# Kernel optimization log

Measured on AMD Instinct MI355X. Metric: run time of the kernel, lower is better.

## Reference

```python
import jax, jax.numpy as jnp
import numpy as np

H, W = 101, 31
HEADS, DH, FREQ = 8, 64, 64
C_DIM = 256
INNER = HEADS * DH
EPS = 1e-5


def _conv2d(x, w, b):
    # x: (B, Cin, H, W), w: (Cout, Cin, 3, 3) -> SAME padding, stride 1
    y = jax.lax.conv_general_dilated(x, w, (1, 1), 'SAME',
                                     dimension_numbers=('NCHW', 'OIHW', 'NCHW'))
    return y + b[None, :, None, None]


def setup_inputs() -> dict:
    key = jax.random.key(0)
    ks = jax.random.split(key, 8)
    B = 32
    N = H * W  # 3131
    s = 0.02
    x = jax.random.normal(ks[0], (B, N, C_DIM), jnp.float32)
    conv_fx_w = jax.random.normal(ks[1], (INNER, C_DIM, 3, 3), jnp.float32) * s
    conv_fx_b = jnp.zeros((INNER,), jnp.float32)
    conv_x_w = jax.random.normal(ks[2], (INNER, C_DIM, 3, 3), jnp.float32) * s
    conv_x_b = jnp.zeros((INNER,), jnp.float32)
    gate_w = jax.random.normal(ks[3], (FREQ, DH), jnp.float32) * s  # nn.Linear weight (out,in)
    gate_b = jnp.zeros((FREQ,), jnp.float32)
    temperature = jnp.full((1, HEADS, 1, 1), 0.5, jnp.float32)
    ln_gamma = jnp.ones((FREQ, DH), jnp.float32)
    ln_beta = jnp.zeros((FREQ, DH), jnp.float32)
    mlp_w = jax.random.normal(ks[4], (DH, DH), jnp.float32) * s
    out_w = jax.random.normal(ks[5], (C_DIM, INNER), jnp.float32) * s
    out_b = jnp.zeros((C_DIM,), jnp.float32)
    # fixed (non-trainable) spectral basis, L2-normalized per row like F.normalize(dim=-1)
    inver = jax.random.normal(ks[6], (N, FREQ), jnp.float32)
    inver = inver / jnp.linalg.norm(inver, axis=-1, keepdims=True)
    return dict(x=x, conv_fx_w=conv_fx_w, conv_fx_b=conv_fx_b, conv_x_w=conv_x_w,
                conv_x_b=conv_x_b, gate_w=gate_w, gate_b=gate_b,
                temperature=temperature, ln_gamma=ln_gamma, ln_beta=ln_beta,
                mlp_w=mlp_w, out_w=out_w, out_b=out_b, inver=inver)


def reference(x, conv_fx_w, conv_fx_b, conv_x_w, conv_x_b, gate_w, gate_b,
              temperature, ln_gamma, ln_beta, mlp_w, out_w, out_b, inver):
    B, N, C = x.shape
    xi = x.reshape(B, H, W, C).transpose(0, 3, 1, 2)  # (B, C, H, W)

    def proj(w, b):
        y = _conv2d(xi, w, b)                                  # (B, inner, H, W)
        return y.transpose(0, 2, 3, 1).reshape(B, N, HEADS, DH).transpose(0, 2, 1, 3)  # (B,h,N,d)

    fx_mid = proj(conv_fx_w, conv_fx_b)
    x_mid = proj(conv_x_w, conv_x_b)

    temp = jnp.clip(temperature, 0.1, 5.0)                      # (1,h,1,1)
    logits = jnp.einsum('bhnc,gc->bhng', x_mid, gate_w) + gate_b
    gate = jax.nn.softmax(logits / temp, axis=-1)               # (B,h,N,g)
    eigens = gate * inver[None, None]                           # (B,h,N,g)

    spec = jnp.einsum('bhnc,bhng->bhgc', fx_mid, eigens)        # (B,h,g,c)
    # LayerNorm over the trailing (g, c) axes jointly
    mu = spec.mean(axis=(-2, -1), keepdims=True)
    var = spec.var(axis=(-2, -1), keepdims=True)
    spec = (spec - mu) * jax.lax.rsqrt(var + EPS) * ln_gamma + ln_beta

    out_spec = jnp.einsum('bhgi,io->bhgo', spec, mlp_w)
    out_x = jnp.einsum('bhgc,bhng->bhnc', out_spec, eigens)     # (B,h,N,c)
    out_x = out_x.transpose(0, 2, 1, 3).reshape(B, N, HEADS * DH)
    return jnp.einsum('bnd,cd->bnc', out_x, out_w) + out_b      # to_out (dropout is identity)
```

## Files before the change

kernel.cpp:

```cpp
#include <hip/hip_runtime.h>
#include <hip/hip_bf16.h>
#include <stdint.h>

#define HH 101
#define WW 31
#define NN 3131
#define NPAD 3136
#define BB 32
#define NH 8
#define CDIM 256
#define GG 64
#define HP 103
#define WP 33

typedef __attribute__((ext_vector_type(8))) short bf16x8;
typedef __attribute__((ext_vector_type(4))) float f32x4;
typedef __attribute__((ext_vector_type(4))) unsigned short ushort4_t;
typedef __attribute__((ext_vector_type(8))) unsigned short ushort8_t;
typedef __attribute__((ext_vector_type(4))) float float4_t;

static __device__ __forceinline__ unsigned short f2bf(float f) {
  union { float f; uint32_t u; } v; v.f = f;
  uint32_t u = v.u;
  return (unsigned short)((u + 0x7fffu + ((u >> 16) & 1u)) >> 16);
}
static __device__ __forceinline__ float bf2f(unsigned short h) {
  union { uint32_t u; float f; } v; v.u = ((uint32_t)h) << 16;
  return v.f;
}
static __device__ __forceinline__ void gload_lds16(const void* g, void* l) {
  __builtin_amdgcn_global_load_lds((const __attribute__((address_space(1))) void*)g,
                                   (__attribute__((address_space(3))) void*)l, 16, 0, 0);
}
static __device__ __forceinline__ int xcd_swz(int bid, int nwg) {
  int q = nwg >> 3, r = nwg & 7;
  int xcd = bid & 7, pos = bid >> 3;
  int base = (xcd < r) ? xcd * (q + 1) : r * (q + 1) + (xcd - r) * q;
  return base + pos;
}

__global__ void k_pad(const float* __restrict__ x, unsigned short* __restrict__ xpad, int b0) {
  const int xx = blockIdx.x, yy = blockIdx.y, b = blockIdx.z;
  const int t = threadIdx.x;
  ushort4_t o; o.x = 0; o.y = 0; o.z = 0; o.w = 0;
  if (yy >= 1 && yy <= HH && xx >= 1 && xx <= WW) {
    const int n = (yy - 1) * WW + (xx - 1);
    const float4_t v = *(const float4_t*)(x + (((int64_t)(b0 + b) * NN + n) * CDIM + t * 4));
    o.x = f2bf(v.x); o.y = f2bf(v.y); o.z = f2bf(v.z); o.w = f2bf(v.w);
  }
  *(ushort4_t*)(xpad + (((int64_t)b * HP + yy) * WP + xx) * CDIM + t * 4) = o;
}

__global__ void k_wpack(const float* __restrict__ fxw, const float* __restrict__ xw,
                        const float* __restrict__ fxb, const float* __restrict__ xb,
                        const float* __restrict__ gw,
                        unsigned short* __restrict__ Wb, float* __restrict__ bias,
                        unsigned short* __restrict__ gwb) {
  int tid = blockIdx.x * blockDim.x + threadIdx.x;
  const int total = 9 * 1024 * 256;
  if (tid < total) {
    int cin = tid & 255; int rest = tid >> 8; int co = rest & 1023; int t = rest >> 10;
    float v = (co < 512) ? fxw[(int64_t)co * 2304 + cin * 9 + t]
                         : xw[(int64_t)(co - 512) * 2304 + cin * 9 + t];
    Wb[tid] = f2bf(v);
  }
  if (tid < 1024) bias[tid] = (tid < 512) ? fxb[tid] : xb[tid - 512];
  if (tid < 4096) gwb[tid] = f2bf(gw[tid]);
}

__global__ void k_pprep(const float* __restrict__ mlp, const float* __restrict__ outw,
                        unsigned short* __restrict__ Pt) {
  int h = blockIdx.x >> 6, i = blockIdx.x & 63, co = threadIdx.x;
  float a = 0.f;
  for (int c = 0; c < 64; ++c) a += mlp[i * 64 + c] * outw[(int64_t)co * 512 + h * 64 + c];
  Pt[((int64_t)h * 256 + co) * 64 + i] = f2bf(a);
}

__global__ void k_padzero(unsigned short* __restrict__ fxT, unsigned short* __restrict__ xmid,
                          int CB) {
  int tid = blockIdx.x * blockDim.x + threadIdx.x;
  if (tid >= CB * 2560) return;
  {
    int j = tid % 5; int rc = tid / 5;
    fxT[(int64_t)rc * NPAD + NN + j] = 0;
  }
  {
    int d = tid & 63; int rest = tid >> 6;
    int j = rest % 5; int bh = rest / 5;
    xmid[((int64_t)bh * NPAD + NN + j) * 64 + d] = 0;
  }
}

__launch_bounds__(512, 2)
__global__ void k_conv8(const unsigned short* __restrict__ xpad,
                        const unsigned short* __restrict__ Wb,
                        const float* __restrict__ bias,
                        unsigned short* __restrict__ fxT,
                        unsigned short* __restrict__ xmid) {
  extern __shared__ unsigned short lds[];
  const int swz = xcd_swz(blockIdx.x, gridDim.x);
  const int r   = swz % 52;
  const int b   = swz / 52;
  const int bx  = r & 3;
  const int mt  = r >> 2;
  const int tid = threadIdx.x, wid = tid >> 6, lane = tid & 63;
  const int wm = wid & 3, wn = wid >> 2;
  const int arow = lane & 15, col16 = lane >> 4;
  const int n00 = mt * 256, co00 = bx * 256;

  const int srow = wid * 16 + (lane >> 2);
  const int tc   = ((lane & 3) ^ ((lane >> 3) & 3)) * 8;
  int na0 = n00 + srow;        if (na0 >= NN) na0 = NN - 1;
  int na1 = n00 + srow + 128;  if (na1 >= NN) na1 = NN - 1;
  const int y0 = na0 / WW, x0v = na0 % WW;
  const int y1 = na1 / WW, x1v = na1 % WW;
  const unsigned short* aS0 = xpad + ((int64_t)(b * HP + y0) * WP + x0v) * CDIM + tc;
  const unsigned short* aS1 = xpad + ((int64_t)(b * HP + y1) * WP + x1v) * CDIM + tc;
  const unsigned short* bS0 = Wb + (int64_t)(co00 + srow) * CDIM + tc;
  const unsigned short* bS1 = Wb + (int64_t)(co00 + srow + 128) * CDIM + tc;

  const int rdsz = (col16 ^ ((arow >> 1) & 3)) * 8;

  f32x4 acc[4][8] = {};
  bf16x8 a0[4], a1[4], b03[4], b47[4];

#define STAGE_A(s, kk, aoffv)                                        \
  { unsigned short* d = lds + (s) * 32768 + (kk) * 8192 + wid * 512; \
    gload_lds16(aS0 + (aoffv) + (kk) * 32, d);                       \
    gload_lds16(aS1 + (aoffv) + (kk) * 32, d + 4096); }
#define STAGE_B(s, kk, boffv)                                                \
  { unsigned short* d = lds + (s) * 32768 + 16384 + (kk) * 8192 + wid * 512; \
    gload_lds16(bS0 + (boffv) + (kk) * 32, d);                               \
    gload_lds16(bS1 + (boffv) + (kk) * 32, d + 4096); }
#define KOFF(ks, aoffv, boffv)                              \
  { const int tap = (ks) >> 2;                              \
    const int dy = (tap >= 6) + (tap >= 3);                 \
    const int dx = tap - dy * 3;                            \
    const int cb = ((ks) & 3) << 6;                         \
    aoffv = (dy * WP + dx) * CDIM + cb;                     \
    boffv = tap * 262144 + cb; }
#define RD_A(dst, s, kk, mf)                                                             \
  dst = *(const bf16x8*)(lds + (s) * 32768 + (kk) * 8192 +                               \
                         (wm * 64 + (mf) * 16 + arow) * 32 + rdsz);
#define RD_B(dst, s, kk, nf)                                                             \
  dst = *(const bf16x8*)(lds + (s) * 32768 + 16384 + (kk) * 8192 +                       \
                         (wn * 128 + (nf) * 16 + arow) * 32 + rdsz);
#define MFMA16(aset, bset, nbase)                                                        \
  __builtin_amdgcn_s_setprio(1);                                                         \
  _Pragma("unroll")                                                                      \
  for (int mf = 0; mf < 4; ++mf) {                                                       \
    _Pragma("unroll")                                                                    \
    for (int nf = 0; nf < 4; ++nf)                                                       \
      acc[mf][(nbase) + nf] =                                                            \
        __builtin_amdgcn_mfma_f32_16x16x32_bf16(aset[mf], bset[nf], acc[mf][(nbase) + nf], 0, 0, 0); \
  }                                                                                      \
  __builtin_amdgcn_s_setprio(0);

  int aoff0, boff0;
  KOFF(0, aoff0, boff0);
  STAGE_A(0, 0, aoff0); STAGE_B(0, 0, boff0);
  STAGE_A(0, 1, aoff0); STAGE_B(0, 1, boff0);
  asm volatile("s_waitcnt vmcnt(4)" ::: "memory");
  __builtin_amdgcn_s_barrier();
  asm volatile("" ::: "memory");
  #pragma unroll
  for (int i = 0; i < 4; ++i) { RD_A(a0[i], 0, 0, i); }
  #pragma unroll
  for (int i = 0; i < 4; ++i) { RD_B(b03[i], 0, 0, i); }

  #pragma unroll 1
  for (int t = 0; t < 36; ++t) {
    const int cur = t & 1, nxt = cur ^ 1;
    const int tn = (t < 35) ? t + 1 : 35;
    int aoffn, boffn;
    KOFF(tn, aoffn, boffn);

    #pragma unroll
    for (int i = 0; i < 4; ++i) { RD_B(b47[i], cur, 0, 4 + i); }
    STAGE_A(nxt, 0, aoffn);
    asm volatile("s_waitcnt lgkmcnt(4)" ::: "memory");
    __builtin_amdgcn_sched_barrier(0);
    MFMA16(a0, b03, 0);

    STAGE_B(nxt, 0, boffn);
    asm volatile("s_waitcnt vmcnt(4)" ::: "memory");
    __builtin_amdgcn_s_barrier();
    asm volatile("" ::: "memory");
    #pragma unroll
    for (int i = 0; i < 4; ++i) { RD_A(a1[i], cur, 1, i); }
    #pragma unroll
    for (int i = 0; i < 4; ++i) { RD_B(b03[i], cur, 1, i); }
    asm volatile("s_waitcnt lgkmcnt(8)" ::: "memory");
    __builtin_amdgcn_sched_barrier(0);
    MFMA16(a0, b47, 4);

    #pragma unroll
    for (int i = 0; i < 4; ++i) { RD_B(b47[i], cur, 1, 4 + i); }
    STAGE_A(nxt, 1, aoffn);
    asm volatile("s_waitcnt lgkmcnt(4)" ::: "memory");
    __builtin_amdgcn_sched_barrier(0);
    MFMA16(a1, b03, 0);

    STAGE_B(nxt, 1, boffn);
    asm volatile("s_waitcnt vmcnt(4)" ::: "memory");
    __builtin_amdgcn_s_barrier();
    asm volatile("" ::: "memory");
    #pragma unroll
    for (int i = 0; i < 4; ++i) { RD_A(a0[i], nxt, 0, i); }
    #pragma unroll
    for (int i = 0; i < 4; ++i) { RD_B(b03[i], nxt, 0, i); }
    asm volatile("s_waitcnt lgkmcnt(8)" ::: "memory");
    __builtin_amdgcn_sched_barrier(0);
    MFMA16(a1, b47, 4);
  }

  asm volatile("s_waitcnt vmcnt(0) lgkmcnt(0)" ::: "memory");

  const int rowoff = col16 * 4;
  #pragma unroll
  for (int mf = 0; mf < 4; ++mf) {
    const int nr = n00 + wm * 64 + mf * 16 + rowoff;
    #pragma unroll
    for (int nf = 0; nf < 8; ++nf) {
      const int co = co00 + wn * 128 + nf * 16 + arow;
      const float bvs = bias[co];
      const float v0 = acc[mf][nf][0] + bvs;
      const float v1 = acc[mf][nf][1] + bvs;
      const float v2 = acc[mf][nf][2] + bvs;
      const float v3 = acc[mf][nf][3] + bvs;
      if (bx < 2) {
        const int h = co >> 6, c = co & 63;
        unsigned short* dst = fxT + ((int64_t)((b * NH + h) * 64 + c)) * NPAD + nr;
        if (nr + 3 < NN) {
          ushort4_t o; o.x = f2bf(v0); o.y = f2bf(v1); o.z = f2bf(v2); o.w = f2bf(v3);
          *(ushort4_t*)dst = o;
        } else {
          if (nr + 0 < NN) dst[0] = f2bf(v0);
          if (nr + 1 < NN) dst[1] = f2bf(v1);
          if (nr + 2 < NN) dst[2] = f2bf(v2);
          if (nr + 3 < NN) dst[3] = f2bf(v3);
        }
      } else {
        const int h = (co >> 6) & 7, d = co & 63;
        unsigned short* dst = xmid + ((int64_t)(b * NH + h) * NPAD + nr) * 64 + d;
        if (nr + 0 < NN) dst[0] = f2bf(v0);
        if (nr + 1 < NN) dst[64] = f2bf(v1);
        if (nr + 2 < NN) dst[128] = f2bf(v2);
        if (nr + 3 < NN) dst[192] = f2bf(v3);
      }
    }
  }
#undef STAGE_A
#undef STAGE_B
#undef KOFF
#undef RD_A
#undef RD_B
#undef MFMA16
}

__global__ void k_eig(const unsigned short* __restrict__ xmid,
                      const unsigned short* __restrict__ gwb,
                      const float* __restrict__ gateb,
                      const float* __restrict__ temperature,
                      const float* __restrict__ inver,
                      unsigned short* __restrict__ eigT,
                      unsigned short* __restrict__ eigN) {
  __shared__ unsigned short egN[64 * 72];
  __shared__ unsigned short egT[64 * 72];
  const int nt = blockIdx.x, h = blockIdx.y, b = blockIdx.z;
  const int tid = threadIdx.x;
  const int w = tid >> 6, lane = tid & 63;
  const int n0 = nt * 64 + w * 16;
  const int bh = b * NH + h;
  float tv = temperature[h];
  tv = fminf(fmaxf(tv, 0.1f), 5.0f);
  const float itemp = 1.0f / tv;
  const int arow = lane & 15;
  const int koff = (lane >> 4) * 8;
  const unsigned short* aptr = xmid + ((int64_t)bh * NPAD + (n0 + arow)) * 64 + koff;
  bf16x8 a0 = *(const bf16x8*)(aptr);
  bf16x8 a1 = *(const bf16x8*)(aptr + 32);
  f32x4 acc[4] = {};
  #pragma unroll
  for (int ng = 0; ng < 4; ++ng) {
    const unsigned short* bptr = gwb + (ng * 16 + arow) * 64 + koff;
    bf16x8 b0 = *(const bf16x8*)(bptr);
    bf16x8 b1 = *(const bf16x8*)(bptr + 32);
    acc[ng] = __builtin_amdgcn_mfma_f32_16x16x32_bf16(a0, b0, acc[ng], 0, 0, 0);
    acc[ng] = __builtin_amdgcn_mfma_f32_16x16x32_bf16(a1, b1, acc[ng], 0, 0, 0);
  }
  #pragma unroll
  for (int r = 0; r < 4; ++r) {
    const int nl = w * 16 + ((lane >> 4) << 2) + r;
    const int n = nt * 64 + nl;
    float vals[4];
    #pragma unroll
    for (int ng = 0; ng < 4; ++ng) vals[ng] = (acc[ng][r] + gateb[ng * 16 + arow]) * itemp;
    float mx = fmaxf(fmaxf(vals[0], vals[1]), fmaxf(vals[2], vals[3]));
    #pragma unroll
    for (int s = 1; s < 16; s <<= 1) mx = fmaxf(mx, __shfl_xor(mx, s));
    float ex[4]; float sum = 0.f;
    #pragma unroll
    for (int ng = 0; ng < 4; ++ng) { ex[ng] = __expf(vals[ng] - mx); sum += ex[ng]; }
    #pragma unroll
    for (int s = 1; s < 16; s <<= 1) sum += __shfl_xor(sum, s);
    const float inv = 1.0f / sum;
    const bool valid = (n < NN);
    #pragma unroll
    for (int ng = 0; ng < 4; ++ng) {
      const int g = ng * 16 + arow;
      float iv = valid ? inver[(int64_t)n * GG + g] : 0.f;
      unsigned short u = valid ? f2bf(ex[ng] * inv * iv) : (unsigned short)0;
      egN[nl * 72 + g] = u;
      egT[g * 72 + nl] = u;
    }
  }
  __syncthreads();
  const int row = tid >> 2, c0 = (tid & 3) << 4;
  {
    ushort8_t v0 = *(ushort8_t*)&egN[row * 72 + c0];
    ushort8_t v1 = *(ushort8_t*)&egN[row * 72 + c0 + 8];
    unsigned short* dst = eigN + ((int64_t)bh * NPAD + nt * 64 + row) * 64 + c0;
    *(ushort8_t*)dst = v0; *(ushort8_t*)(dst + 8) = v1;
  }
  {
    ushort8_t v0 = *(ushort8_t*)&egT[row * 72 + c0];
    ushort8_t v1 = *(ushort8_t*)&egT[row * 72 + c0 + 8];
    unsigned short* dst = eigT + ((int64_t)(bh * 64 + row)) * NPAD + nt * 64 + c0;
    *(ushort8_t*)dst = v0; *(ushort8_t*)(dst + 8) = v1;
  }
}

__launch_bounds__(256, 1)
__global__ void k_specln(const unsigned short* __restrict__ eigT,
                         const unsigned short* __restrict__ fxT,
                         const float* __restrict__ gamma, const float* __restrict__ beta,
                         const unsigned short* __restrict__ Pt,
                         unsigned short* __restrict__ m2t) {
  extern __shared__ char sm[];
  float* sacc = (float*)sm;
  unsigned short* specb = (unsigned short*)(sm + 66560);
  float* red = (float*)(sm + 74752);
  unsigned short* mstrip = (unsigned short*)(sm + 74784);
  const int bhl = blockIdx.x;
  const int h = bhl & 7, bl = bhl >> 3;
  const int tid = threadIdx.x, w = tid >> 6, lane = tid & 63;
  const int arow = lane & 15, col16 = lane >> 4;
  const int koff = col16 * 8;
  const unsigned short* eb = eigT + (int64_t)bhl * 64 * NPAD;
  const unsigned short* fb = fxT + (int64_t)bhl * 64 * NPAD;

  const int ks0 = (98 * w) >> 2, ks1 = (98 * (w + 1)) >> 2;
  f32x4 acc[4][4] = {};
  for (int ks = ks0; ks < ks1; ++ks) {
    const int k0 = ks * 32 + koff;
    bf16x8 av[4], bv[4];
    #pragma unroll
    for (int mg = 0; mg < 4; ++mg) av[mg] = *(const bf16x8*)(eb + (int64_t)(mg * 16 + arow) * NPAD + k0);
    #pragma unroll
    for (int ng = 0; ng < 4; ++ng) bv[ng] = *(const bf16x8*)(fb + (int64_t)(ng * 16 + arow) * NPAD + k0);
    #pragma unroll
    for (int mg = 0; mg < 4; ++mg)
      #pragma unroll
      for (int ng = 0; ng < 4; ++ng)
        acc[mg][ng] = __builtin_amdgcn_mfma_f32_16x16x32_bf16(av[mg], bv[ng], acc[mg][ng], 0, 0, 0);
  }
  float* pw = sacc + w * (64 * 65);
  #pragma unroll
  for (int mg = 0; mg < 4; ++mg)
    #pragma unroll
    for (int ng = 0; ng < 4; ++ng)
      #pragma unroll
      for (int r = 0; r < 4; ++r)
        pw[(mg * 16 + col16 * 4 + r) * 65 + ng * 16 + arow] = acc[mg][ng][r];
  __syncthreads();

  float vloc[16];
  float lsum = 0.f, lsq = 0.f;
  #pragma unroll
  for (int idx = 0; idx < 16; ++idx) {
    const int e = tid + idx * 256;
    const int g = e >> 6, c = e & 63;
    float v = sacc[g * 65 + c] + sacc[4160 + g * 65 + c] +
              sacc[8320 + g * 65 + c] + sacc[12480 + g * 65 + c];
    vloc[idx] = v; lsum += v; lsq += v * v;
  }
  #pragma unroll
  for (int s = 1; s < 64; s <<= 1) { lsum += __shfl_xor(lsum, s); lsq += __shfl_xor(lsq, s); }
  if (lane == 0) { red[w] = lsum; red[4 + w] = lsq; }
  __syncthreads();
  const float tsum = red[0] + red[1] + red[2] + red[3];
  const float tsq = red[4] + red[5] + red[6] + red[7];
  const float mu = tsum * (1.0f / 4096.0f);
  const float var = tsq * (1.0f / 4096.0f) - mu * mu;
  const float rs = rsqrtf(var + 1e-5f);
  #pragma unroll
  for (int idx = 0; idx < 16; ++idx) {
    const int e = tid + idx * 256;
    const int g = e >> 6, c = e & 63;
    float sv = (vloc[idx] - mu) * rs * gamma[e] + beta[e];
    specb[g * 64 + ((((c >> 3) ^ (g & 7))) << 3) + (c & 7)] = f2bf(sv);
  }
  __syncthreads();

  f32x4 a2[4][4] = {};
  const unsigned short* pth = Pt + ((int64_t)h * 256 + w * 64) * 64;
  #pragma unroll
  for (int kk = 0; kk < 2; ++kk) {
    const int i0 = kk * 32 + koff;
    const int i8 = (i0 >> 3);
    bf16x8 av2[4], bv2[4];
    #pragma unroll
    for (int mg = 0; mg < 4; ++mg) {
      const int g = mg * 16 + arow;
      av2[mg] = *(const bf16x8*)(specb + g * 64 + ((i8 ^ (g & 7)) << 3));
    }
    #pragma unroll
    for (int ng = 0; ng < 4; ++ng)
      bv2[ng] = *(const bf16x8*)(pth + (ng * 16 + arow) * 64 + i0);
    #pragma unroll
    for (int mg = 0; mg < 4; ++mg)
      #pragma unroll
      for (int ng = 0; ng < 4; ++ng)
        a2[mg][ng] = __builtin_amdgcn_mfma_f32_16x16x32_bf16(av2[mg], bv2[ng], a2[mg][ng], 0, 0, 0);
  }
  unsigned short* ms = mstrip + w * (64 * 72);
  #pragma unroll
  for (int mg = 0; mg < 4; ++mg)
    #pragma unroll
    for (int ng = 0; ng < 4; ++ng)
      #pragma unroll
      for (int r = 0; r < 4; ++r)
        ms[(ng * 16 + arow) * 72 + mg * 16 + col16 * 4 + r] = f2bf(a2[mg][ng][r]);
  __syncthreads();
  #pragma unroll
  for (int e0 = 0; e0 < 8; ++e0) {
    const int e = lane + e0 * 64;
    const int row = e >> 3, g8 = e & 7;
    ushort8_t v = *(ushort8_t*)&ms[row * 72 + g8 * 8];
    *(ushort8_t*)(m2t + ((int64_t)(bl * 256 + w * 64 + row)) * 512 + h * 64 + g8 * 8) = v;
  }
}

__launch_bounds__(256)
__global__ void k_out(const unsigned short* __restrict__ eigN,
                      const unsigned short* __restrict__ m2t,
                      const float* __restrict__ outb,
                      float* __restrict__ out, int b0) {
  const int swz = xcd_swz(blockIdx.x, gridDim.x);
  const int ct = swz & 1;
  const int mt = (swz >> 1) % 25;
  const int b  = swz / 50;
  const int w = threadIdx.x >> 6, lane = threadIdx.x & 63;
  const int wm = w >> 1, wn = w & 1;
  const int arow = lane & 15, koff = (lane >> 4) * 8;
  const int co0 = ct * 128 + wn * 64;
  const int n0 = mt * 128 + wm * 64;
  f32x4 acc[4][4] = {};
  const unsigned short* ebase = eigN + (int64_t)b * NH * NPAD * 64;
  const unsigned short* mbase = m2t + (int64_t)b * 256 * 512;
  for (int ks = 0; ks < 16; ++ks) {
    const int hh = ks >> 1;
    const int g0 = (ks & 1) * 32 + koff;
    bf16x8 av[4], bv[4];
    #pragma unroll
    for (int mg = 0; mg < 4; ++mg) {
      int n = n0 + mg * 16 + arow;
      if (n > NPAD - 1) n = NPAD - 1;
      av[mg] = *(const bf16x8*)(ebase + ((int64_t)hh * NPAD + n) * 64 + g0);
    }
    #pragma unroll
    for (int ng = 0; ng < 4; ++ng)
      bv[ng] = *(const bf16x8*)(mbase + (int64_t)(co0 + ng * 16 + arow) * 512 + ks * 32 + koff);
    #pragma unroll
    for (int mg = 0; mg < 4; ++mg)
      #pragma unroll
      for (int ng = 0; ng < 4; ++ng)
        acc[mg][ng] = __builtin_amdgcn_mfma_f32_16x16x32_bf16(av[mg], bv[ng], acc[mg][ng], 0, 0, 0);
  }
  #pragma unroll
  for (int mg = 0; mg < 4; ++mg) {
    const int nr = n0 + mg * 16 + ((lane >> 4) << 2);
    #pragma unroll
    for (int ng = 0; ng < 4; ++ng) {
      const int co = co0 + ng * 16 + arow;
      const float bv = outb[co];
      #pragma unroll
      for (int r = 0; r < 4; ++r) {
        if (nr + r < NN)
          out[((int64_t)(b0 + b) * NN + nr + r) * 256 + co] = acc[mg][ng][r] + bv;
      }
    }
  }
}

extern "C" void kernel_launch(void* const* d_in, const int* in_sizes, int n_in,
                              void* d_out, int out_size, void* d_ws, size_t ws_size,
                              hipStream_t stream) {
  const float* x     = (const float*)d_in[0];
  const float* fxw   = (const float*)d_in[1];
  const float* fxb   = (const float*)d_in[2];
  const float* xw    = (const float*)d_in[3];
  const float* xb    = (const float*)d_in[4];
  const float* gw    = (const float*)d_in[5];
  const float* gb    = (const float*)d_in[6];
  const float* temp  = (const float*)d_in[7];
  const float* gamma = (const float*)d_in[8];
  const float* beta  = (const float*)d_in[9];
  const float* mlp   = (const float*)d_in[10];
  const float* outw  = (const float*)d_in[11];
  const float* outb  = (const float*)d_in[12];
  const float* inver = (const float*)d_in[13];
  float* out = (float*)d_out;
  char* ws = (char*)d_ws;
  (void)in_sizes; (void)n_in; (void)out_size;

  hipFuncSetAttribute(reinterpret_cast<const void*>(k_conv8),
                      hipFuncAttributeMaxDynamicSharedMemorySize, 131072);
  hipFuncSetAttribute(reinterpret_cast<const void*>(k_specln),
                      hipFuncAttributeMaxDynamicSharedMemorySize, 131072);

  int CB = 1;
  {
    const int cands[6] = {32, 16, 8, 4, 2, 1};
    for (int i = 0; i < 6; ++i) {
      unsigned long long need = 4993024ull + (unsigned long long)cands[i] * 14847488ull;
      if (need <= (unsigned long long)ws_size) { CB = cands[i]; break; }
    }
  }

  unsigned short* Wb   = (unsigned short*)(ws + 0);
  float*          bias = (float*)(ws + 4718592);
  unsigned short* gwb  = (unsigned short*)(ws + 4722688);
  unsigned short* Pt   = (unsigned short*)(ws + 4730880);
  const size_t F0      = 4993024;
  const size_t szXpad  = (size_t)CB * 1740288;
  const size_t szM2t   = (size_t)CB * 262144;
  const size_t szBig   = (size_t)CB * 3211264;
  unsigned short* xpad = (unsigned short*)(ws + F0);
  unsigned short* m2t  = (unsigned short*)(ws + F0 + szXpad);
  unsigned short* fxT  = (unsigned short*)(ws + F0 + szXpad + szM2t);
  unsigned short* xmid = (unsigned short*)(ws + F0 + szXpad + szM2t + szBig);
  unsigned short* eigT = (unsigned short*)(ws + F0 + szXpad + szM2t + 2 * szBig);
  unsigned short* eigN = (unsigned short*)(ws + F0 + szXpad + szM2t + 3 * szBig);

  k_wpack<<<dim3(9216), dim3(256), 0, stream>>>(fxw, xw, fxb, xb, gw, Wb, bias, gwb);
  k_pprep<<<dim3(512), dim3(256), 0, stream>>>(mlp, outw, Pt);

  for (int b0 = 0; b0 < BB; b0 += CB) {
    k_pad<<<dim3(WP, HP, CB), dim3(64), 0, stream>>>(x, xpad, b0);
    k_padzero<<<dim3(CB * 10), dim3(256), 0, stream>>>(fxT, xmid, CB);
    k_conv8<<<dim3(52 * CB), dim3(512), 131072, stream>>>(xpad, Wb, bias, fxT, xmid);
    k_eig<<<dim3(49, 8, CB), dim3(256), 0, stream>>>(xmid, gwb, gb, temp, inver, eigT, eigN);
    k_specln<<<dim3(CB * 8), dim3(256), 111648, stream>>>(eigT, fxT, gamma, beta, Pt, m2t);
    k_out<<<dim3(50 * CB), dim3(256), 0, stream>>>(eigN, m2t, outb, out, b0);
  }
}
```

Baseline: 884.9 us.

## Split spectral GEMM into split-K partial kernel plus separate LayerNorm/MLP kernel

The fused spectral kernel, which ran one block per (batch, head), becomes two kernels. The first computes split-K partial products across twice as many blocks and writes fp32 partials to the workspace, reusing the xpad region. The second reduces those partials and then applies LayerNorm and the MLP. This raises parallelism in the K-reduction GEMM and drops the large dynamic shared memory allocation, at the cost of a global round-trip for the partials and an extra launch. The largest chunk size is also capped at 16, because the partial buffer must fit inside the xpad region.

```diff
diff --git a/kernel.cpp b/kernel.cpp
--- a/kernel.cpp
+++ b/kernel.cpp
@@ -331,58 +331,63 @@
   }
 }
 
-__launch_bounds__(256, 1)
-__global__ void k_specln(const unsigned short* __restrict__ eigT,
-                         const unsigned short* __restrict__ fxT,
-                         const float* __restrict__ gamma, const float* __restrict__ beta,
-                         const unsigned short* __restrict__ Pt,
-                         unsigned short* __restrict__ m2t) {
-  extern __shared__ char sm[];
-  float* sacc = (float*)sm;
-  unsigned short* specb = (unsigned short*)(sm + 66560);
-  float* red = (float*)(sm + 74752);
-  unsigned short* mstrip = (unsigned short*)(sm + 74784);
+__global__ void k_specA(const unsigned short* __restrict__ eigT,
+                        const unsigned short* __restrict__ fxT,
+                        float* __restrict__ part) {
+  const int q = blockIdx.x, bhl = blockIdx.y;
+  const int tid = threadIdx.x, w = tid >> 6, lane = tid & 63;
+  const int s = q * 4 + w;
+  const int ks0 = (98 * s) >> 3, ks1 = (98 * (s + 1)) >> 3;
+  const int arow = lane & 15, col16 = lane >> 4;
+  const int koff = col16 * 8;
+  const unsigned short* eb = eigT + (int64_t)bhl * 64 * NPAD;
+  const unsigned short* fb = fxT + (int64_t)bhl * 64 * NPAD;
+  f32x4 acc[4][4] = {};
+  for (int ks = ks0; ks < ks1; ++ks) {
+    const int k0 = ks * 32 + koff;
+    bf16x8 av[4], bv[4];
+    #pragma unroll
+    for (int mg = 0; mg < 4; ++mg) av[mg] = *(const bf16x8*)(eb + (int64_t)(mg * 16 + arow) * NPAD + k0);
+    #pragma unroll
+    for (int ng = 0; ng < 4; ++ng) bv[ng] = *(const bf16x8*)(fb + (int64_t)(ng * 16 + arow) * NPAD + k0);
+    #pragma unroll
+    for (int mg = 0; mg < 4; ++mg)
+      #pragma unroll
+      for (int ng = 0; ng < 4; ++ng)
+        acc[mg][ng] = __builtin_amdgcn_mfma_f32_16x16x32_bf16(av[mg], bv[ng], acc[mg][ng], 0, 0, 0);
+  }
+  float* pb = part + ((int64_t)bhl * 8 + s) * 4096;
+  #pragma unroll
+  for (int mg = 0; mg < 4; ++mg)
+    #pragma unroll
+    for (int ng = 0; ng < 4; ++ng)
+      #pragma unroll
+      for (int r = 0; r < 4; ++r)
+        pb[(mg * 16 + col16 * 4 + r) * 64 + ng * 16 + arow] = acc[mg][ng][r];
+}
+
+__global__ void k_specB(const float* __restrict__ part,
+                        const float* __restrict__ gamma, const float* __restrict__ beta,
+                        const unsigned short* __restrict__ Pt,
+                        unsigned short* __restrict__ m2t) {
+  __shared__ unsigned short specb[64 * 64];
+  __shared__ float red[8];
+  __shared__ unsigned short mstrip[4 * 64 * 72];
   const int bhl = blockIdx.x;
   const int h = bhl & 7, bl = bhl >> 3;
   const int tid = threadIdx.x, w = tid >> 6, lane = tid & 63;
   const int arow = lane & 15, col16 = lane >> 4;
   const int koff = col16 * 8;
-  const unsigned short* eb = eigT + (int64_t)bhl * 64 * NPAD;
-  const unsigned short* fb = fxT + (int64_t)bhl * 64 * NPAD;
-
-  const int ks0 = (98 * w) >> 2, ks1 = (98 * (w + 1)) >> 2;
-  f32x4 acc[4][4] = {};
-  for (int ks = ks0; ks < ks1; ++ks) {
-    const int k0 = ks * 32 + koff;
-    bf16x8 av[4], bv[4];
-    #pragma unroll
-    for (int mg = 0; mg < 4; ++mg) av[mg] = *(const bf16x8*)(eb + (int64_t)(mg * 16 + arow) * NPAD + k0);
-    #pragma unroll
-    for (int ng = 0; ng < 4; ++ng) bv[ng] = *(const bf16x8*)(fb + (int64_t)(ng * 16 + arow) * NPAD + k0);
-    #pragma unroll
-    for (int mg = 0; mg < 4; ++mg)
-      #pragma unroll
-      for (int ng = 0; ng < 4; ++ng)
-        acc[mg][ng] = __builtin_amdgcn_mfma_f32_16x16x32_bf16(av[mg], bv[ng], acc[mg][ng], 0, 0, 0);
-  }
-  float* pw = sacc + w * (64 * 65);
-  #pragma unroll
-  for (int mg = 0; mg < 4; ++mg)
-    #pragma unroll
-    for (int ng = 0; ng < 4; ++ng)
-      #pragma unroll
-      for (int r = 0; r < 4; ++r)
-        pw[(mg * 16 + col16 * 4 + r) * 65 + ng * 16 + arow] = acc[mg][ng][r];
-  __syncthreads();
+  const float* pb = part + (int64_t)bhl * 8 * 4096;
 
   float vloc[16];
   float lsum = 0.f, lsq = 0.f;
   #pragma unroll
   for (int idx = 0; idx < 16; ++idx) {
     const int e = tid + idx * 256;
-    const int g = e >> 6, c = e & 63;
-    float v = sacc[g * 65 + c] + sacc[4160 + g * 65 + c] +
-              sacc[8320 + g * 65 + c] + sacc[12480 + g * 65 + c];
+    float v = 0.f;
+    #pragma unroll
+    for (int s = 0; s < 8; ++s) v += pb[s * 4096 + e];
     vloc[idx] = v; lsum += v; lsq += v * v;
   }
   #pragma unroll
@@ -517,13 +522,11 @@
 
   hipFuncSetAttribute(reinterpret_cast<const void*>(k_conv8),
                       hipFuncAttributeMaxDynamicSharedMemorySize, 131072);
-  hipFuncSetAttribute(reinterpret_cast<const void*>(k_specln),
-                      hipFuncAttributeMaxDynamicSharedMemorySize, 131072);
 
   int CB = 1;
   {
-    const int cands[6] = {32, 16, 8, 4, 2, 1};
-    for (int i = 0; i < 6; ++i) {
+    const int cands[5] = {16, 8, 4, 2, 1};
+    for (int i = 0; i < 5; ++i) {
       unsigned long long need = 4993024ull + (unsigned long long)cands[i] * 14847488ull;
       if (need <= (unsigned long long)ws_size) { CB = cands[i]; break; }
     }
@@ -538,6 +541,7 @@
   const size_t szM2t   = (size_t)CB * 262144;
   const size_t szBig   = (size_t)CB * 3211264;
   unsigned short* xpad = (unsigned short*)(ws + F0);
+  float*          part = (float*)(ws + F0);
   unsigned short* m2t  = (unsigned short*)(ws + F0 + szXpad);
   unsigned short* fxT  = (unsigned short*)(ws + F0 + szXpad + szM2t);
   unsigned short* xmid = (unsigned short*)(ws + F0 + szXpad + szM2t + szBig);
@@ -552,7 +556,8 @@
     k_padzero<<<dim3(CB * 10), dim3(256), 0, stream>>>(fxT, xmid, CB);
     k_conv8<<<dim3(52 * CB), dim3(512), 131072, stream>>>(xpad, Wb, bias, fxT, xmid);
     k_eig<<<dim3(49, 8, CB), dim3(256), 0, stream>>>(xmid, gwb, gb, temp, inver, eigT, eigN);
-    k_specln<<<dim3(CB * 8), dim3(256), 111648, stream>>>(eigT, fxT, gamma, beta, Pt, m2t);
+    k_specA<<<dim3(2, CB * 8), dim3(256), 0, stream>>>(eigT, fxT, part);
+    k_specB<<<dim3(CB * 8), dim3(256), 0, stream>>>(part, gamma, beta, Pt, m2t);
     k_out<<<dim3(50 * CB), dim3(256), 0, stream>>>(eigN, m2t, outb, out, b0);
   }
 }
```

Result: no change. 889.3 us (+0.5%).
